# Kernel tuning notes

Measured on AMD Instinct MI355X. Metric: run time of the kernel, lower is better.

## Reference

```python
import jax, jax.numpy as jnp
import numpy as np

N_ATOMS = 50000
N_PAIRS = 800000
N_EMB = 128
N_DIST = 100
N_HID = 128


def _glorot(key, shape):
    scale = jnp.sqrt(2.0 / (shape[0] + shape[1])).astype(jnp.float32)
    return jax.random.normal(key, shape, dtype=jnp.float32) * scale


def setup_inputs() -> dict:
    key = jax.random.key(0)
    ks = jax.random.split(key, 10)
    atom_features = jax.random.normal(ks[0], (N_ATOMS, N_EMB), dtype=jnp.float32)
    distance = jax.random.uniform(ks[1], (N_PAIRS, N_DIST), dtype=jnp.float32)
    atom_membership = jax.random.randint(ks[2], (N_ATOMS,), 0, 64, dtype=jnp.int32)
    distance_membership_i = jnp.sort(
        jax.random.randint(ks[3], (N_PAIRS,), 0, N_ATOMS, dtype=jnp.int32))
    distance_membership_j = jax.random.randint(ks[4], (N_PAIRS,), 0, N_ATOMS, dtype=jnp.int32)
    W_cf = _glorot(ks[5], (N_EMB, N_HID))
    W_df = _glorot(ks[6], (N_DIST, N_HID))
    W_fc = _glorot(ks[7], (N_HID, N_EMB))
    # original inits biases to zero; use small random so the b_df*afh branch is non-trivial
    b_cf = jax.random.normal(ks[8], (N_HID,), dtype=jnp.float32) * 0.1
    b_df = jax.random.normal(ks[9], (N_HID,), dtype=jnp.float32) * 0.1
    return {
        "atom_features": atom_features,
        "distance": distance,
        "atom_membership": atom_membership,
        "distance_membership_i": distance_membership_i,
        "distance_membership_j": distance_membership_j,
        "W_cf": W_cf, "W_df": W_df, "W_fc": W_fc,
        "b_cf": b_cf, "b_df": b_df,
    }


def reference(atom_features, distance, atom_membership,
              distance_membership_i, distance_membership_j,
              W_cf, W_df, W_fc, b_cf, b_df):
    n_atoms = atom_features.shape[0]
    # [n_pairs, n_hidden]
    distance_hidden = distance @ W_df + b_df
    # [n_atoms, n_hidden]
    atom_features_hidden = atom_features @ W_cf + b_cf
    # gather source-atom hidden feats per pair, fuse with distance feats
    msgs = distance_hidden * atom_features_hidden[distance_membership_j]
    msgs = jnp.tanh(msgs @ W_fc)                      # [n_pairs, n_emb]
    # self-interaction correction term
    output_ii = jnp.tanh((b_df * atom_features_hidden) @ W_fc)  # [n_atoms, n_emb]
    agg = jax.ops.segment_sum(msgs, distance_membership_i, num_segments=n_atoms)
    return agg - output_ii + atom_features
```

## Files before the change

kernel.cpp:

```cpp
#include <hip/hip_runtime.h>
#include <hip/hip_bf16.h>

#define N_ATOMS 50000
#define N_PAIRS 800000
#define N_EMB   128
#define N_DIST  100
#define N_HID   128
#define TP      128

typedef __attribute__((ext_vector_type(8))) short bf16x8;
typedef __attribute__((ext_vector_type(4))) float f32x4;

__device__ __forceinline__ short f2b(float x) {
  union { float f; unsigned u; } v; v.f = x;
  unsigned r = (v.u + 0x7FFF + ((v.u >> 16) & 1)) >> 16;
  return (short)r;
}
__device__ __forceinline__ float b2f(short b) {
  union { unsigned u; float f; } v; v.u = ((unsigned)(unsigned short)b) << 16;
  return v.f;
}
__device__ __forceinline__ float fast_tanh(float x) {
  const float z = __builtin_amdgcn_exp2f(x * 2.8853900817779268f);
  return 1.f - 2.f * __builtin_amdgcn_rcpf(z + 1.f);
}

__device__ __forceinline__ int frag_idx(int k, int n) {
  return ((((k >> 5) * 8 + (n >> 4)) * 64) + (((k >> 3) & 3) * 16) + (n & 15)) * 8 + (k & 7);
}

__device__ __forceinline__ void g2lds16(const void* g, void* l) {
  __builtin_amdgcn_global_load_lds(
      (const __attribute__((address_space(1))) unsigned*)g,
      (__attribute__((address_space(3))) unsigned*)l, 16, 0, 0);
}
__device__ __forceinline__ void stage_weights(const short* __restrict__ src,
                                              short* WS, int tid) {
  #pragma unroll
  for (int r = 0; r < 4; ++r) {
    const int off = (r * 512 + tid) * 8;
    g2lds16(src + off, WS + off);
  }
}

__global__ __launch_bounds__(256) void prep_kernel(
    const float* __restrict__ Wcf, const float* __restrict__ Wdf,
    const float* __restrict__ Wfc, short* __restrict__ Wcf_f,
    short* __restrict__ Wdf_f, short* __restrict__ Wfc_f) {
  const int e = blockIdx.x * 256 + threadIdx.x;
  const int k = e >> 7, n = e & 127;
  const int fi = frag_idx(k, n);
  Wcf_f[fi] = f2b(Wcf[k * N_HID + n]);
  Wfc_f[fi] = f2b(Wfc[k * N_EMB + n]);
  Wdf_f[fi] = (k < N_DIST) ? f2b(Wdf[k * N_HID + n]) : (short)0;
}

__global__ __launch_bounds__(512) void afh_kernel(
    const float* __restrict__ af, const short* __restrict__ Wcf_f,
    const float* __restrict__ bcf, float* __restrict__ afh) {
  __shared__ short WS[128 * 128];
  const int tid = threadIdx.x;
  const int lane = tid & 63, w = tid >> 6;
  const int lane15 = lane & 15, quad = lane >> 4;
  const int a0 = blockIdx.x * 128;

  stage_weights(Wcf_f, WS, tid);

  f32x4 acc[8];
  #pragma unroll
  for (int nt = 0; nt < 8; ++nt) {
    const float b = bcf[nt * 16 + lane15];
    acc[nt] = (f32x4){b, b, b, b};
  }
  const int arow = min(a0 + w * 16 + lane15, N_ATOMS - 1);
  const float* __restrict__ p = af + (long)arow * N_EMB;
  __syncthreads();

  for (int ks = 0; ks < 4; ++ks) {
    const int k0 = ks * 32 + quad * 8;
    const float4 x = *(const float4*)(p + k0);
    const float4 y = *(const float4*)(p + k0 + 4);
    bf16x8 a;
    a[0] = f2b(x.x); a[1] = f2b(x.y); a[2] = f2b(x.z); a[3] = f2b(x.w);
    a[4] = f2b(y.x); a[5] = f2b(y.y); a[6] = f2b(y.z); a[7] = f2b(y.w);
    #pragma unroll
    for (int nt = 0; nt < 8; ++nt) {
      const bf16x8 b = *(const bf16x8*)&WS[((ks * 8 + nt) * 64 + lane) * 8];
      acc[nt] = __builtin_amdgcn_mfma_f32_16x16x32_bf16(a, b, acc[nt], 0, 0, 0);
    }
  }
  #pragma unroll
  for (int reg = 0; reg < 4; ++reg) {
    const int row = a0 + w * 16 + quad * 4 + reg;
    if (row < N_ATOMS) {
      #pragma unroll
      for (int nt = 0; nt < 8; ++nt)
        afh[(long)row * N_HID + nt * 16 + lane15] = acc[nt][reg];
    }
  }
}

__global__ __launch_bounds__(512, 4) void pair_kernel(
    const float* __restrict__ dist, const int* __restrict__ mi,
    const int* __restrict__ mj, const short* __restrict__ Wdf_f,
    const short* __restrict__ Wfc_f, const float* __restrict__ bdf,
    const float* __restrict__ afh, float* __restrict__ agg) {
  __shared__ short WS[128 * 128];
  __shared__ short HS[TP * 128];

  const int tid = threadIdx.x;
  const int lane = tid & 63;
  const int w = tid >> 6;
  const int lane15 = lane & 15;
  const int quad = lane >> 4;
  const long pbase = (long)blockIdx.x * TP;
  const int R = w * 16;

  stage_weights(Wdf_f, WS, tid);

  float g[4][8];
  #pragma unroll
  for (int reg = 0; reg < 4; ++reg) {
    const int r = R + quad * 4 + reg;
    const long j = mj[pbase + r];
    const float* __restrict__ arow = afh + j * N_HID + lane15;
    #pragma unroll
    for (int nt = 0; nt < 8; ++nt)
      g[reg][nt] = arow[nt * 16];
  }

  const float* __restrict__ drow = dist + (pbase + R + lane15) * (long)N_DIST;
  float4 dx[4], dy[4];
  #pragma unroll
  for (int ks = 0; ks < 3; ++ks) {
    const int k0 = ks * 32 + quad * 8;
    dx[ks] = *(const float4*)(drow + k0);
    dy[ks] = *(const float4*)(drow + k0 + 4);
  }
  {
    const float4 z = {0.f, 0.f, 0.f, 0.f};
    dx[3] = (quad == 0) ? *(const float4*)(drow + 96) : z;
    dy[3] = z;
  }

  f32x4 acc[8];
  #pragma unroll
  for (int nt = 0; nt < 8; ++nt) {
    const float b = bdf[nt * 16 + lane15];
    acc[nt] = (f32x4){b, b, b, b};
  }
  __syncthreads();

  #pragma unroll
  for (int ks = 0; ks < 4; ++ks) {
    bf16x8 a;
    a[0] = f2b(dx[ks].x); a[1] = f2b(dx[ks].y);
    a[2] = f2b(dx[ks].z); a[3] = f2b(dx[ks].w);
    a[4] = f2b(dy[ks].x); a[5] = f2b(dy[ks].y);
    a[6] = f2b(dy[ks].z); a[7] = f2b(dy[ks].w);
    #pragma unroll
    for (int nt = 0; nt < 8; ++nt) {
      const bf16x8 b = *(const bf16x8*)&WS[((ks * 8 + nt) * 64 + lane) * 8];
      acc[nt] = __builtin_amdgcn_mfma_f32_16x16x32_bf16(a, b, acc[nt], 0, 0, 0);
    }
  }
  __syncthreads();

  stage_weights(Wfc_f, WS, tid);

  #pragma unroll
  for (int reg = 0; reg < 4; ++reg) {
    const int r = R + quad * 4 + reg;
    #pragma unroll
    for (int nt = 0; nt < 8; ++nt) {
      const int col = nt * 16 + lane15;
      const float h = acc[nt][reg] * g[reg][nt];
      const int ch = (col >> 3) ^ (r & 15);
      HS[(r << 7) + (ch << 3) + (col & 7)] = f2b(h);
    }
  }
  __syncthreads();

  f32x4 acc2[8];
  #pragma unroll
  for (int nt = 0; nt < 8; ++nt) acc2[nt] = (f32x4){0.f, 0.f, 0.f, 0.f};
  const int m = R + lane15;
  #pragma unroll
  for (int ks = 0; ks < 4; ++ks) {
    const int ch = (ks * 4 + quad) ^ lane15;
    const bf16x8 a = *(const bf16x8*)&HS[(m << 7) + (ch << 3)];
    #pragma unroll
    for (int nt = 0; nt < 8; ++nt) {
      const bf16x8 b = *(const bf16x8*)&WS[((ks * 8 + nt) * 64 + lane) * 8];
      acc2[nt] = __builtin_amdgcn_mfma_f32_16x16x32_bf16(a, b, acc2[nt], 0, 0, 0);
    }
  }

  #pragma unroll
  for (int reg = 0; reg < 4; ++reg) {
    const int r = R + quad * 4 + reg;
    #pragma unroll
    for (int nt = 0; nt < 8; ++nt) {
      const int col = nt * 16 + lane15;
      const float tv = fast_tanh(acc2[nt][reg]);
      const int ch = (col >> 3) ^ (r & 15);
      HS[(r << 7) + (ch << 3) + (col & 7)] = f2b(tv);
    }
  }
  __builtin_amdgcn_wave_barrier();

  {
    const int c0 = lane * 2;
    const long p0 = pbase + R;
    float s0 = 0.f, s1 = 0.f;
    int cur = mi[p0];
    for (int rr = 0; rr < 16; ++rr) {
      const int r = R + rr;
      const int idx = mi[p0 + rr];
      if (idx != cur) {
        atomicAdd(&agg[(size_t)cur * N_EMB + c0], s0);
        atomicAdd(&agg[(size_t)cur * N_EMB + c0 + 1], s1);
        s0 = s1 = 0.f; cur = idx;
      }
      const int ch = (c0 >> 3) ^ (r & 15);
      const unsigned v =
          *(const unsigned*)&HS[(r << 7) + (ch << 3) + (c0 & 7)];
      s0 += b2f((short)(v & 0xFFFF));
      s1 += b2f((short)(v >> 16));
    }
    atomicAdd(&agg[(size_t)cur * N_EMB + c0], s0);
    atomicAdd(&agg[(size_t)cur * N_EMB + c0 + 1], s1);
  }
}

__global__ __launch_bounds__(512) void out_kernel(
    const float* __restrict__ af, const float* __restrict__ afh,
    const short* __restrict__ Wfc_f, const float* __restrict__ bdf,
    const float* __restrict__ agg, float* __restrict__ out) {
  __shared__ short WS[128 * 128];
  const int tid = threadIdx.x;
  const int lane = tid & 63, w = tid >> 6;
  const int lane15 = lane & 15, quad = lane >> 4;
  const int a0 = blockIdx.x * 128;

  stage_weights(Wfc_f, WS, tid);

  f32x4 acc[8];
  #pragma unroll
  for (int nt = 0; nt < 8; ++nt) acc[nt] = (f32x4){0.f, 0.f, 0.f, 0.f};
  const int arow = min(a0 + w * 16 + lane15, N_ATOMS - 1);
  const float* __restrict__ p = afh + (long)arow * N_HID;
  __syncthreads();

  for (int ks = 0; ks < 4; ++ks) {
    const int k0 = ks * 32 + quad * 8;
    const float4 x = *(const float4*)(p + k0);
    const float4 y = *(const float4*)(p + k0 + 4);
    const float4 bx = *(const float4*)(bdf + k0);
    const float4 by = *(const float4*)(bdf + k0 + 4);
    bf16x8 a;
    a[0] = f2b(x.x * bx.x); a[1] = f2b(x.y * bx.y);
    a[2] = f2b(x.z * bx.z); a[3] = f2b(x.w * bx.w);
    a[4] = f2b(y.x * by.x); a[5] = f2b(y.y * by.y);
    a[6] = f2b(y.z * by.z); a[7] = f2b(y.w * by.w);
    #pragma unroll
    for (int nt = 0; nt < 8; ++nt) {
      const bf16x8 b = *(const bf16x8*)&WS[((ks * 8 + nt) * 64 + lane) * 8];
      acc[nt] = __builtin_amdgcn_mfma_f32_16x16x32_bf16(a, b, acc[nt], 0, 0, 0);
    }
  }
  #pragma unroll
  for (int reg = 0; reg < 4; ++reg) {
    const int row = a0 + w * 16 + quad * 4 + reg;
    if (row < N_ATOMS) {
      #pragma unroll
      for (int nt = 0; nt < 8; ++nt) {
        const size_t idx = (size_t)row * N_EMB + nt * 16 + lane15;
        out[idx] = agg[idx] - fast_tanh(acc[nt][reg]) + af[idx];
      }
    }
  }
}

extern "C" void kernel_launch(void* const* d_in, const int* in_sizes, int n_in,
                              void* d_out, int out_size, void* d_ws, size_t ws_size,
                              hipStream_t stream) {
  const float* af   = (const float*)d_in[0];
  const float* dist = (const float*)d_in[1];
  const int*   mi   = (const int*)d_in[3];
  const int*   mj   = (const int*)d_in[4];
  const float* Wcf  = (const float*)d_in[5];
  const float* Wdf  = (const float*)d_in[6];
  const float* Wfc  = (const float*)d_in[7];
  const float* bcf  = (const float*)d_in[8];
  const float* bdf  = (const float*)d_in[9];
  float* out = (float*)d_out;

  float* afh = (float*)d_ws;
  float* agg = afh + (size_t)N_ATOMS * N_HID;
  short* Wcf_f = (short*)(agg + (size_t)N_ATOMS * N_EMB);
  short* Wdf_f = Wcf_f + 128 * 128;
  short* Wfc_f = Wdf_f + 128 * 128;

  hipMemsetAsync(agg, 0, (size_t)N_ATOMS * N_EMB * sizeof(float), stream);
  prep_kernel<<<64, 256, 0, stream>>>(Wcf, Wdf, Wfc, Wcf_f, Wdf_f, Wfc_f);
  afh_kernel<<<(N_ATOMS + 127) / 128, 512, 0, stream>>>(af, Wcf_f, bcf, afh);
  pair_kernel<<<N_PAIRS / TP, 512, 0, stream>>>(dist, mi, mj, Wdf_f, Wfc_f, bdf, afh, agg);
  out_kernel<<<(N_ATOMS + 127) / 128, 512, 0, stream>>>(af, afh, Wfc_f, bdf, agg, out);
}
```

Before: 601.5 us.

## Make pair kernel persistent with per-wave strips and double-buffered prefetch

The pair kernel becomes persistent: 250 blocks, and each wave handles 25 consecutive strips of 16 pairs. Both weight matrices are staged into LDS once per block instead of once per 128 pairs. Each wave prefetches the next strip's distance rows and gathered atom features into registers while it computes the current strip. The segment-sum running accumulator carries across strips, which cuts down on atomics. In exchange, register pressure rises (launch bounds drop to 2 blocks per CU) and only 250 blocks run, so the load may be unbalanced across the GPU's compute units.

```diff
diff --git a/kernel.cpp b/kernel.cpp
--- a/kernel.cpp
+++ b/kernel.cpp
@@ -6,7 +6,8 @@
 #define N_EMB   128
 #define N_DIST  100
 #define N_HID   128
-#define TP      128
+#define NB      250
+#define SPW     25
 
 typedef __attribute__((ext_vector_type(8))) short bf16x8;
 typedef __attribute__((ext_vector_type(4))) float f32x4;
@@ -100,137 +101,161 @@
   }
 }
 
-__global__ __launch_bounds__(512, 4) void pair_kernel(
+struct Pref {
+  float4 x[4];
+  float4 y[3];
+  float  g[4][8];
+};
+
+__device__ __forceinline__ void prefetch_strip(
+    const float* __restrict__ dist, const int* __restrict__ mj,
+    const float* __restrict__ afh, long p0, int lane15, int quad, Pref& P) {
+  const float* __restrict__ drow = dist + (p0 + lane15) * (long)N_DIST;
+  #pragma unroll
+  for (int ks = 0; ks < 3; ++ks) {
+    const int k0 = ks * 32 + quad * 8;
+    P.x[ks] = *(const float4*)(drow + k0);
+    P.y[ks] = *(const float4*)(drow + k0 + 4);
+  }
+  const float4 z = {0.f, 0.f, 0.f, 0.f};
+  P.x[3] = (quad == 0) ? *(const float4*)(drow + 96) : z;
+  #pragma unroll
+  for (int reg = 0; reg < 4; ++reg) {
+    const long j = mj[p0 + quad * 4 + reg];
+    const float* __restrict__ arow = afh + j * N_HID + lane15;
+    #pragma unroll
+    for (int nt = 0; nt < 8; ++nt) P.g[reg][nt] = arow[nt * 16];
+  }
+}
+
+__device__ __forceinline__ void compute_strip(
+    const Pref& P, const short* WS, short* HSw, const float* bv,
+    int lane, int lane15, int quad, const int* __restrict__ mi, long p0,
+    int& cur, float& s0, float& s1, float* __restrict__ agg, int c0) {
+  bf16x8 afr[4];
+  #pragma unroll
+  for (int ks = 0; ks < 3; ++ks) {
+    afr[ks][0] = f2b(P.x[ks].x); afr[ks][1] = f2b(P.x[ks].y);
+    afr[ks][2] = f2b(P.x[ks].z); afr[ks][3] = f2b(P.x[ks].w);
+    afr[ks][4] = f2b(P.y[ks].x); afr[ks][5] = f2b(P.y[ks].y);
+    afr[ks][6] = f2b(P.y[ks].z); afr[ks][7] = f2b(P.y[ks].w);
+  }
+  afr[3][0] = f2b(P.x[3].x); afr[3][1] = f2b(P.x[3].y);
+  afr[3][2] = f2b(P.x[3].z); afr[3][3] = f2b(P.x[3].w);
+  afr[3][4] = 0; afr[3][5] = 0; afr[3][6] = 0; afr[3][7] = 0;
+
+  f32x4 acc[8];
+  #pragma unroll
+  for (int nt = 0; nt < 8; ++nt)
+    acc[nt] = (f32x4){bv[nt], bv[nt], bv[nt], bv[nt]};
+  #pragma unroll
+  for (int ks = 0; ks < 4; ++ks) {
+    #pragma unroll
+    for (int nt = 0; nt < 8; ++nt) {
+      const bf16x8 b = *(const bf16x8*)&WS[((ks * 8 + nt) * 64 + lane) * 8];
+      acc[nt] = __builtin_amdgcn_mfma_f32_16x16x32_bf16(afr[ks], b, acc[nt], 0, 0, 0);
+    }
+  }
+
+  #pragma unroll
+  for (int reg = 0; reg < 4; ++reg) {
+    const int r = quad * 4 + reg;
+    #pragma unroll
+    for (int nt = 0; nt < 8; ++nt) {
+      const int col = nt * 16 + lane15;
+      const float h = acc[nt][reg] * P.g[reg][nt];
+      const int ch = (col >> 3) ^ r;
+      HSw[(r << 7) + (ch << 3) + (col & 7)] = f2b(h);
+    }
+  }
+  __builtin_amdgcn_wave_barrier();
+
+  f32x4 acc2[8];
+  #pragma unroll
+  for (int nt = 0; nt < 8; ++nt) acc2[nt] = (f32x4){0.f, 0.f, 0.f, 0.f};
+  #pragma unroll
+  for (int ks = 0; ks < 4; ++ks) {
+    const int ch = (ks * 4 + quad) ^ lane15;
+    const bf16x8 a = *(const bf16x8*)&HSw[(lane15 << 7) + (ch << 3)];
+    #pragma unroll
+    for (int nt = 0; nt < 8; ++nt) {
+      const bf16x8 b = *(const bf16x8*)&WS[16384 + ((ks * 8 + nt) * 64 + lane) * 8];
+      acc2[nt] = __builtin_amdgcn_mfma_f32_16x16x32_bf16(a, b, acc2[nt], 0, 0, 0);
+    }
+  }
+
+  #pragma unroll
+  for (int reg = 0; reg < 4; ++reg) {
+    const int r = quad * 4 + reg;
+    #pragma unroll
+    for (int nt = 0; nt < 8; ++nt) {
+      const int col = nt * 16 + lane15;
+      const float tv = fast_tanh(acc2[nt][reg]);
+      const int ch = (col >> 3) ^ r;
+      HSw[(r << 7) + (ch << 3) + (col & 7)] = f2b(tv);
+    }
+  }
+  __builtin_amdgcn_wave_barrier();
+
+  for (int rr = 0; rr < 16; ++rr) {
+    const int idx = mi[p0 + rr];
+    if (idx != cur) {
+      atomicAdd(&agg[(size_t)cur * N_EMB + c0], s0);
+      atomicAdd(&agg[(size_t)cur * N_EMB + c0 + 1], s1);
+      s0 = s1 = 0.f; cur = idx;
+    }
+    const int ch = (c0 >> 3) ^ rr;
+    const unsigned v =
+        *(const unsigned*)&HSw[(rr << 7) + (ch << 3) + (c0 & 7)];
+    s0 += b2f((short)(v & 0xFFFF));
+    s1 += b2f((short)(v >> 16));
+  }
+}
+
+__global__ __launch_bounds__(512, 2) void pair_kernel(
     const float* __restrict__ dist, const int* __restrict__ mi,
     const int* __restrict__ mj, const short* __restrict__ Wdf_f,
     const short* __restrict__ Wfc_f, const float* __restrict__ bdf,
     const float* __restrict__ afh, float* __restrict__ agg) {
-  __shared__ short WS[128 * 128];
-  __shared__ short HS[TP * 128];
+  __shared__ short WS[2 * 128 * 128];
+  __shared__ short HS[8 * 16 * 128];
 
   const int tid = threadIdx.x;
   const int lane = tid & 63;
   const int w = tid >> 6;
   const int lane15 = lane & 15;
   const int quad = lane >> 4;
-  const long pbase = (long)blockIdx.x * TP;
-  const int R = w * 16;
 
   stage_weights(Wdf_f, WS, tid);
-
-  float g[4][8];
-  #pragma unroll
-  for (int reg = 0; reg < 4; ++reg) {
-    const int r = R + quad * 4 + reg;
-    const long j = mj[pbase + r];
-    const float* __restrict__ arow = afh + j * N_HID + lane15;
-    #pragma unroll
-    for (int nt = 0; nt < 8; ++nt)
-      g[reg][nt] = arow[nt * 16];
-  }
-
-  const float* __restrict__ drow = dist + (pbase + R + lane15) * (long)N_DIST;
-  float4 dx[4], dy[4];
-  #pragma unroll
-  for (int ks = 0; ks < 3; ++ks) {
-    const int k0 = ks * 32 + quad * 8;
-    dx[ks] = *(const float4*)(drow + k0);
-    dy[ks] = *(const float4*)(drow + k0 + 4);
-  }
-  {
-    const float4 z = {0.f, 0.f, 0.f, 0.f};
-    dx[3] = (quad == 0) ? *(const float4*)(drow + 96) : z;
-    dy[3] = z;
-  }
-
-  f32x4 acc[8];
-  #pragma unroll
-  for (int nt = 0; nt < 8; ++nt) {
-    const float b = bdf[nt * 16 + lane15];
-    acc[nt] = (f32x4){b, b, b, b};
-  }
+  stage_weights(Wfc_f, WS + 16384, tid);
+
+  float bv[8];
+  #pragma unroll
+  for (int nt = 0; nt < 8; ++nt) bv[nt] = bdf[nt * 16 + lane15];
+
+  short* HSw = HS + w * 2048;
+  const long wbase = ((long)blockIdx.x * 8 + w) * (SPW * 16);
+  const int c0 = lane * 2;
   __syncthreads();
 
-  #pragma unroll
-  for (int ks = 0; ks < 4; ++ks) {
-    bf16x8 a;
-    a[0] = f2b(dx[ks].x); a[1] = f2b(dx[ks].y);
-    a[2] = f2b(dx[ks].z); a[3] = f2b(dx[ks].w);
-    a[4] = f2b(dy[ks].x); a[5] = f2b(dy[ks].y);
-    a[6] = f2b(dy[ks].z); a[7] = f2b(dy[ks].w);
-    #pragma unroll
-    for (int nt = 0; nt < 8; ++nt) {
-      const bf16x8 b = *(const bf16x8*)&WS[((ks * 8 + nt) * 64 + lane) * 8];
-      acc[nt] = __builtin_amdgcn_mfma_f32_16x16x32_bf16(a, b, acc[nt], 0, 0, 0);
-    }
-  }
-  __syncthreads();
-
-  stage_weights(Wfc_f, WS, tid);
-
-  #pragma unroll
-  for (int reg = 0; reg < 4; ++reg) {
-    const int r = R + quad * 4 + reg;
-    #pragma unroll
-    for (int nt = 0; nt < 8; ++nt) {
-      const int col = nt * 16 + lane15;
-      const float h = acc[nt][reg] * g[reg][nt];
-      const int ch = (col >> 3) ^ (r & 15);
-      HS[(r << 7) + (ch << 3) + (col & 7)] = f2b(h);
-    }
-  }
-  __syncthreads();
-
-  f32x4 acc2[8];
-  #pragma unroll
-  for (int nt = 0; nt < 8; ++nt) acc2[nt] = (f32x4){0.f, 0.f, 0.f, 0.f};
-  const int m = R + lane15;
-  #pragma unroll
-  for (int ks = 0; ks < 4; ++ks) {
-    const int ch = (ks * 4 + quad) ^ lane15;
-    const bf16x8 a = *(const bf16x8*)&HS[(m << 7) + (ch << 3)];
-    #pragma unroll
-    for (int nt = 0; nt < 8; ++nt) {
-      const bf16x8 b = *(const bf16x8*)&WS[((ks * 8 + nt) * 64 + lane) * 8];
-      acc2[nt] = __builtin_amdgcn_mfma_f32_16x16x32_bf16(a, b, acc2[nt], 0, 0, 0);
-    }
-  }
-
-  #pragma unroll
-  for (int reg = 0; reg < 4; ++reg) {
-    const int r = R + quad * 4 + reg;
-    #pragma unroll
-    for (int nt = 0; nt < 8; ++nt) {
-      const int col = nt * 16 + lane15;
-      const float tv = fast_tanh(acc2[nt][reg]);
-      const int ch = (col >> 3) ^ (r & 15);
-      HS[(r << 7) + (ch << 3) + (col & 7)] = f2b(tv);
-    }
-  }
-  __builtin_amdgcn_wave_barrier();
-
-  {
-    const int c0 = lane * 2;
-    const long p0 = pbase + R;
-    float s0 = 0.f, s1 = 0.f;
-    int cur = mi[p0];
-    for (int rr = 0; rr < 16; ++rr) {
-      const int r = R + rr;
-      const int idx = mi[p0 + rr];
-      if (idx != cur) {
-        atomicAdd(&agg[(size_t)cur * N_EMB + c0], s0);
-        atomicAdd(&agg[(size_t)cur * N_EMB + c0 + 1], s1);
-        s0 = s1 = 0.f; cur = idx;
-      }
-      const int ch = (c0 >> 3) ^ (r & 15);
-      const unsigned v =
-          *(const unsigned*)&HS[(r << 7) + (ch << 3) + (c0 & 7)];
-      s0 += b2f((short)(v & 0xFFFF));
-      s1 += b2f((short)(v >> 16));
-    }
-    atomicAdd(&agg[(size_t)cur * N_EMB + c0], s0);
-    atomicAdd(&agg[(size_t)cur * N_EMB + c0 + 1], s1);
-  }
+  Pref pa, pb;
+  prefetch_strip(dist, mj, afh, wbase, lane15, quad, pa);
+  int cur = mi[wbase];
+  float s0 = 0.f, s1 = 0.f;
+
+  #pragma unroll 1
+  for (int s = 0; s < SPW - 1; s += 2) {
+    prefetch_strip(dist, mj, afh, wbase + (s + 1) * 16, lane15, quad, pb);
+    compute_strip(pa, WS, HSw, bv, lane, lane15, quad, mi, wbase + s * 16,
+                  cur, s0, s1, agg, c0);
+    prefetch_strip(dist, mj, afh, wbase + (s + 2) * 16, lane15, quad, pa);
+    compute_strip(pb, WS, HSw, bv, lane, lane15, quad, mi, wbase + (s + 1) * 16,
+                  cur, s0, s1, agg, c0);
+  }
+  compute_strip(pa, WS, HSw, bv, lane, lane15, quad, mi, wbase + (SPW - 1) * 16,
+                cur, s0, s1, agg, c0);
+  atomicAdd(&agg[(size_t)cur * N_EMB + c0], s0);
+  atomicAdd(&agg[(size_t)cur * N_EMB + c0 + 1], s1);
 }
 
 __global__ __launch_bounds__(512) void out_kernel(
@@ -305,6 +330,6 @@
   hipMemsetAsync(agg, 0, (size_t)N_ATOMS * N_EMB * sizeof(float), stream);
   prep_kernel<<<64, 256, 0, stream>>>(Wcf, Wdf, Wfc, Wcf_f, Wdf_f, Wfc_f);
   afh_kernel<<<(N_ATOMS + 127) / 128, 512, 0, stream>>>(af, Wcf_f, bcf, afh);
-  pair_kernel<<<N_PAIRS / TP, 512, 0, stream>>>(dist, mi, mj, Wdf_f, Wfc_f, bdf, afh, agg);
+  pair_kernel<<<NB, 512, 0, stream>>>(dist, mi, mj, Wdf_f, Wfc_f, bdf, afh, agg);
   out_kernel<<<(N_ATOMS + 127) / 128, 512, 0, stream>>>(af, afh, Wfc_f, bdf, agg, out);
 }
```

Measured after the change: 608.6 us. No clear change (+1.2%).
